# Kernel tuning notes

Measured on AMD Instinct MI355X. Metric: run time of the kernel, lower is better.

Reference implementation:

```python
import jax, jax.numpy as jnp
import numpy as np


def setup_inputs() -> dict:
    key = jax.random.key(0)
    k1, k2, k3 = jax.random.split(key, 3)
    B, S, D = 4, 2048, 1024   # batch, seq_len, hidden
    M = 65536                 # external memory size
    x = jax.random.normal(k1, (B, S, D), dtype=jnp.float32)
    keys = jax.random.normal(k2, (M, D), dtype=jnp.float32)
    vals = jax.random.normal(k3, (M, D), dtype=jnp.float32)
    return {"x": x, "ver": 1, "keys": keys, "vals": vals}


def reference(x, ver, keys, vals):
    # linear_attention: unnormalized attention over external memory.
    #   out = (x @ keys^T) @ vals
    # Use associativity to avoid materializing the [B,S,M] score matrix:
    #   kv = keys^T @ vals  -> [D, D]
    kv = jnp.einsum("md,me->de", keys, vals)   # [D, D]
    out = jnp.einsum("bsd,de->bse", x, kv)      # [B, S, D]
    return out
```

## Files before the change

### kernel.cpp

```cpp
#include <hip/hip_runtime.h>
#include <hip/hip_bf16.h>


typedef __attribute__((ext_vector_type(8))) __bf16 bf16x8;
typedef __attribute__((ext_vector_type(4))) __bf16 bf16x4;
typedef __attribute__((ext_vector_type(4))) float  f32x4;

#define D_DIM   1024
#define M_DIM   65536
#define ROWS    8192
#define NCHUNK  16
#define MC      (M_DIM / NCHUNK)
#define BT      128
#define BK      64
#define LDK     72
#define TILE_BYTES 16384

__device__ __forceinline__ f32x4 mfma16(bf16x8 a, bf16x8 b, f32x4 c) {
    return __builtin_amdgcn_mfma_f32_16x16x32_bf16(a, b, c, 0, 0, 0);
}

__device__ __forceinline__ void gl_lds16(const void* gsrc, void* ldst) {
    __builtin_amdgcn_global_load_lds(
        (const __attribute__((address_space(1))) unsigned int*)gsrc,
        (__attribute__((address_space(3))) unsigned int*)ldst,
        16, 0, 0);
}

__global__ __launch_bounds__(256)
void convert_tile(const float* __restrict__ keys,
                  const float* __restrict__ vals,
                  __hip_bfloat16* __restrict__ KtT,
                  __hip_bfloat16* __restrict__ VtT)
{
    __shared__ __bf16 Lt[128][72];

    const float* src = blockIdx.z ? vals : keys;
    char* dstb = (char*)(blockIdx.z ? VtT : KtT);

    const int tid = threadIdx.x;
    const int s  = blockIdx.x;
    const int t  = blockIdx.y;
    const int m0 = s * 64;
    const int d0 = t * 128;

    #pragma unroll
    for (int i = 0; i < 8; ++i) {
        const int idx = tid + i * 256;
        const int mr  = idx >> 5;
        const int dc  = (idx & 31) * 4;
        f32x4 v = *(const f32x4*)(src + (size_t)(m0 + mr) * D_DIM + d0 + dc);
        #pragma unroll
        for (int j = 0; j < 4; ++j)
            Lt[dc + j][mr] = (__bf16)v[j];
    }
    __syncthreads();

    char* dst_tile = dstb + ((size_t)t * 1024 + s) * TILE_BYTES;
    #pragma unroll
    for (int r = 0; r < 4; ++r) {
        const int o  = r * 4096 + tid * 16;
        const int dl = o >> 7;
        const int c  = (o >> 4) & 7;
        const int cl = c ^ (dl & 7);
        bf16x8 w = *(const bf16x8*)&Lt[dl][cl * 8];
        *(bf16x8*)(dst_tile + o) = w;
    }
}

__global__ __launch_bounds__(256)
void kv_gemm(const __hip_bfloat16* __restrict__ VtT,
             const __hip_bfloat16* __restrict__ KtT,
             float* __restrict__ kvw)
{
    __shared__ __bf16 Va[128][64];
    __shared__ __bf16 Ka[128][64];

    const int tid  = threadIdx.x;
    const int lane = tid & 63;
    const int wave = tid >> 6;
    const int wr   = wave >> 1;
    const int wc   = wave & 1;

    const int i64   = blockIdx.x & 63;
    const int chunk = blockIdx.x >> 6;
    const int xcd   = i64 & 7;
    const int slot  = i64 >> 3;
    const int e8 = (xcd >> 1) * 2 + (slot >> 2);
    const int d8 = (xcd & 1) * 4 + (slot & 3);

    const char* srcV = (const char*)VtT
        + ((size_t)e8 * 1024 + (size_t)chunk * 64) * TILE_BYTES
        + wave * 4096 + lane * 16;
    const char* srcK = (const char*)KtT
        + ((size_t)d8 * 1024 + (size_t)chunk * 64) * TILE_BYTES
        + wave * 4096 + lane * 16;
    char* dstV = (char*)&Va[0][0] + wave * 4096;
    char* dstK = (char*)&Ka[0][0] + wave * 4096;

    f32x4 acc[4][4] = {};

    const int l15 = lane & 15;
    const int l7  = lane & 7;
    const int hi  = lane >> 4;

    for (int it = 0; it < 64; ++it) {
        #pragma unroll
        for (int i = 0; i < 4; ++i) {
            gl_lds16(srcV + i * 1024, dstV + i * 1024);
            gl_lds16(srcK + i * 1024, dstK + i * 1024);
        }
        __syncthreads();

        const char* vbase = (const char*)&Va[0][0];
        const char* kbase = (const char*)&Ka[0][0];
        #pragma unroll
        for (int ks = 0; ks < BK; ks += 32) {
            bf16x8 af[4], bf[4];
            const int ca = (ks >> 3) + hi;
            const int pc = (ca ^ l7) << 4;
            #pragma unroll
            for (int tt = 0; tt < 4; ++tt) {
                const int ra = wr * 64 + tt * 16 + l15;
                const int rb = wc * 64 + tt * 16 + l15;
                af[tt] = *(const bf16x8*)(vbase + ra * 128 + pc);
                bf[tt] = *(const bf16x8*)(kbase + rb * 128 + pc);
            }
            #pragma unroll
            for (int mi = 0; mi < 4; ++mi)
                #pragma unroll
                for (int ni = 0; ni < 4; ++ni)
                    acc[mi][ni] = mfma16(af[mi], bf[ni], acc[mi][ni]);
        }
        __syncthreads();

        srcV += TILE_BYTES;
        srcK += TILE_BYTES;
    }

    const int rbase = (lane >> 4) * 4;
    const int cidx  = lane & 15;
    #pragma unroll
    for (int mi = 0; mi < 4; ++mi) {
        #pragma unroll
        for (int ni = 0; ni < 4; ++ni) {
            const int d = d8 * BT + wc * 64 + ni * 16 + cidx;
            #pragma unroll
            for (int reg = 0; reg < 4; ++reg) {
                const int e = e8 * BT + wr * 64 + mi * 16 + rbase + reg;
                atomicAdd(kvw + (size_t)e * D_DIM + d, acc[mi][ni][reg]);
            }
        }
    }
}

__global__ __launch_bounds__(256)
void kv_partial_kernel(const float* __restrict__ keys,
                       const float* __restrict__ vals,
                       float* __restrict__ kvw)
{
    __shared__ __bf16 Ktl[BT][LDK];
    __shared__ __bf16 Vtl[BT][LDK];

    const int tid  = threadIdx.x;
    const int lane = tid & 63;
    const int wave = tid >> 6;
    const int wr   = wave >> 1;
    const int wc   = wave & 1;

    const int tile  = blockIdx.x & 63;
    const int chunk = blockIdx.x >> 6;
    const int d0 = (tile >> 3) * BT;
    const int e0 = (tile & 7) * BT;
    const size_t mbeg = (size_t)chunk * MC;

    f32x4 acc[4][4] = {};
    const int kg  = tid & 15;
    const int d4a = tid >> 4;

    for (int ms = 0; ms < MC; ms += BK) {
        #pragma unroll
        for (int i = 0; i < 2; ++i) {
            const int dloc = (d4a + i * 16) * 4;
            const size_t mrow = mbeg + ms + (size_t)kg * 4;
            f32x4 kr[4], vr[4];
            #pragma unroll
            for (int r = 0; r < 4; ++r) {
                kr[r] = *(const f32x4*)(keys + (mrow + r) * D_DIM + d0 + dloc);
                vr[r] = *(const f32x4*)(vals + (mrow + r) * D_DIM + e0 + dloc);
            }
            #pragma unroll
            for (int j = 0; j < 4; ++j) {
                bf16x4 wk, wv;
                #pragma unroll
                for (int r = 0; r < 4; ++r) {
                    wk[r] = (__bf16)kr[r][j];
                    wv[r] = (__bf16)vr[r][j];
                }
                *(bf16x4*)&Ktl[dloc + j][kg * 4] = wk;
                *(bf16x4*)&Vtl[dloc + j][kg * 4] = wv;
            }
        }
        __syncthreads();

        #pragma unroll
        for (int ks = 0; ks < BK; ks += 32) {
            bf16x8 af[4], bf[4];
            #pragma unroll
            for (int t = 0; t < 4; ++t) {
                af[t] = *(const bf16x8*)&Ktl[wr * 64 + t * 16 + (lane & 15)][ks + (lane >> 4) * 8];
                bf[t] = *(const bf16x8*)&Vtl[wc * 64 + t * 16 + (lane & 15)][ks + (lane >> 4) * 8];
            }
            #pragma unroll
            for (int mi = 0; mi < 4; ++mi)
                #pragma unroll
                for (int ni = 0; ni < 4; ++ni)
                    acc[mi][ni] = mfma16(af[mi], bf[ni], acc[mi][ni]);
        }
        __syncthreads();
    }

    const int rbase = (lane >> 4) * 4;
    const int cidx  = lane & 15;
    #pragma unroll
    for (int mi = 0; mi < 4; ++mi) {
        #pragma unroll
        for (int ni = 0; ni < 4; ++ni) {
            const int e = e0 + wc * 64 + ni * 16 + cidx;
            #pragma unroll
            for (int reg = 0; reg < 4; ++reg) {
                const int d = d0 + wr * 64 + mi * 16 + rbase + reg;
                atomicAdd(kvw + (size_t)e * D_DIM + d, acc[mi][ni][reg]);
            }
        }
    }
}

__global__ __launch_bounds__(256)
void out_gemm_kernel(const float* __restrict__ x,
                     const float* __restrict__ kvw,
                     float* __restrict__ out)
{
    __shared__ __bf16 Xt[BT][LDK];
    __shared__ __bf16 Wt[BT][LDK];

    const int tid  = threadIdx.x;
    const int lane = tid & 63;
    const int wave = tid >> 6;
    const int wr   = wave >> 1;
    const int wc   = wave & 1;

    const int r0 = blockIdx.x * BT;
    const int e0 = blockIdx.y * BT;

    f32x4 acc[4][4] = {};

    for (int ks0 = 0; ks0 < D_DIM; ks0 += BK) {
        #pragma unroll
        for (int i = 0; i < 8; ++i) {
            const int idx = tid + i * 256;
            const int row = idx >> 4;
            const int col = (idx & 15) * 4;
            f32x4 xa = *(const f32x4*)(x   + (size_t)(r0 + row) * D_DIM + ks0 + col);
            f32x4 wa = *(const f32x4*)(kvw + (size_t)(e0 + row) * D_DIM + ks0 + col);
            bf16x4 xb, wb;
            #pragma unroll
            for (int j = 0; j < 4; ++j) {
                xb[j] = (__bf16)xa[j];
                wb[j] = (__bf16)wa[j];
            }
            *(bf16x4*)&Xt[row][col] = xb;
            *(bf16x4*)&Wt[row][col] = wb;
        }
        __syncthreads();

        #pragma unroll
        for (int ks = 0; ks < BK; ks += 32) {
            bf16x8 af[4], bf[4];
            #pragma unroll
            for (int t = 0; t < 4; ++t) {
                af[t] = *(const bf16x8*)&Xt[wr * 64 + t * 16 + (lane & 15)][ks + (lane >> 4) * 8];
                bf[t] = *(const bf16x8*)&Wt[wc * 64 + t * 16 + (lane & 15)][ks + (lane >> 4) * 8];
            }
            #pragma unroll
            for (int mi = 0; mi < 4; ++mi)
                #pragma unroll
                for (int ni = 0; ni < 4; ++ni)
                    acc[mi][ni] = mfma16(af[mi], bf[ni], acc[mi][ni]);
        }
        __syncthreads();
    }

    const int rbase = (lane >> 4) * 4;
    const int cidx  = lane & 15;
    #pragma unroll
    for (int mi = 0; mi < 4; ++mi) {
        #pragma unroll
        for (int ni = 0; ni < 4; ++ni) {
            const int e = e0 + wc * 64 + ni * 16 + cidx;
            #pragma unroll
            for (int reg = 0; reg < 4; ++reg) {
                const int r = r0 + wr * 64 + mi * 16 + rbase + reg;
                out[(size_t)r * D_DIM + e] = acc[mi][ni][reg];
            }
        }
    }
}

extern "C" void kernel_launch(void* const* d_in, const int* in_sizes, int n_in,
                              void* d_out, int out_size, void* d_ws, size_t ws_size,
                              hipStream_t stream) {
    const float* x    = (const float*)d_in[0];
    const float* keys = (const float*)d_in[2];
    const float* vals = (const float*)d_in[3];
    float* out = (float*)d_out;

    const size_t kvw_bytes = (size_t)D_DIM * D_DIM * sizeof(float);
    const size_t kt_bytes  = (size_t)D_DIM * M_DIM * sizeof(__hip_bfloat16);
    const size_t need      = kvw_bytes + 2 * kt_bytes;

    float* kvw = (float*)d_ws;
    hipMemsetAsync(kvw, 0, kvw_bytes, stream);

    if (ws_size >= need) {
        __hip_bfloat16* KtT = (__hip_bfloat16*)((char*)d_ws + kvw_bytes);
        __hip_bfloat16* VtT = (__hip_bfloat16*)((char*)d_ws + kvw_bytes + kt_bytes);
        convert_tile<<<dim3(M_DIM / 64, D_DIM / 128, 2), dim3(256), 0, stream>>>(
            keys, vals, KtT, VtT);
        kv_gemm<<<dim3(64 * NCHUNK), dim3(256), 0, stream>>>(VtT, KtT, kvw);
    } else {
        kv_partial_kernel<<<dim3(64 * NCHUNK), dim3(256), 0, stream>>>(keys, vals, kvw);
    }
    out_gemm_kernel<<<dim3(64, 8), dim3(256), 0, stream>>>(x, kvw, out);
}
```

Before: 425.9 us.

## Double-buffer LDS tiles in kv_gemm to overlap global loads with MFMA

Shared-memory tiles for V and K are doubled so the next K-step's global-to-LDS loads are issued before computing on the current buffer. A partial vmcnt wait (allowing the 8 newest loads in flight) plus raw s_barrier replaces the full __syncthreads, aiming to hide memory latency behind MFMA work. This doubles LDS use to 64 KB per block, which may reduce occupancy. Correctness relies on hand-written waitcnt and barrier ordering.

```diff
diff --git a/kernel.cpp b/kernel.cpp
--- a/kernel.cpp
+++ b/kernel.cpp
@@ -73,8 +73,8 @@
              const __hip_bfloat16* __restrict__ KtT,
              float* __restrict__ kvw)
 {
-    __shared__ __bf16 Va[128][64];
-    __shared__ __bf16 Ka[128][64];
+    __shared__ __bf16 Va[2][128][64];
+    __shared__ __bf16 Ka[2][128][64];
 
     const int tid  = threadIdx.x;
     const int lane = tid & 63;
@@ -95,8 +95,6 @@
     const char* srcK = (const char*)KtT
         + ((size_t)d8 * 1024 + (size_t)chunk * 64) * TILE_BYTES
         + wave * 4096 + lane * 16;
-    char* dstV = (char*)&Va[0][0] + wave * 4096;
-    char* dstK = (char*)&Ka[0][0] + wave * 4096;
 
     f32x4 acc[4][4] = {};
 
@@ -104,16 +102,31 @@
     const int l7  = lane & 7;
     const int hi  = lane >> 4;
 
-    for (int it = 0; it < 64; ++it) {
+    auto stage = [&](int buf, int t) {
+        const char* sv = srcV + (size_t)t * TILE_BYTES;
+        const char* sk = srcK + (size_t)t * TILE_BYTES;
+        char* dv = (char*)&Va[buf][0][0] + wave * 4096;
+        char* dk = (char*)&Ka[buf][0][0] + wave * 4096;
         #pragma unroll
         for (int i = 0; i < 4; ++i) {
-            gl_lds16(srcV + i * 1024, dstV + i * 1024);
-            gl_lds16(srcK + i * 1024, dstK + i * 1024);
-        }
-        __syncthreads();
-
-        const char* vbase = (const char*)&Va[0][0];
-        const char* kbase = (const char*)&Ka[0][0];
+            gl_lds16(sv + i * 1024, dv + i * 1024);
+            gl_lds16(sk + i * 1024, dk + i * 1024);
+        }
+    };
+
+    stage(0, 0);
+
+    for (int t = 0; t < 64; ++t) {
+        if (t + 1 < 64) {
+            stage((t + 1) & 1, t + 1);
+            asm volatile("s_waitcnt vmcnt(8)" ::: "memory");
+        } else {
+            asm volatile("s_waitcnt vmcnt(0)" ::: "memory");
+        }
+        __builtin_amdgcn_s_barrier();
+
+        const char* vbase = (const char*)&Va[t & 1][0][0];
+        const char* kbase = (const char*)&Ka[t & 1][0][0];
         #pragma unroll
         for (int ks = 0; ks < BK; ks += 32) {
             bf16x8 af[4], bf[4];
@@ -132,10 +145,7 @@
                 for (int ni = 0; ni < 4; ++ni)
                     acc[mi][ni] = mfma16(af[mi], bf[ni], acc[mi][ni]);
         }
-        __syncthreads();
-
-        srcV += TILE_BYTES;
-        srcK += TILE_BYTES;
+        __builtin_amdgcn_s_barrier();
     }
 
     const int rbase = (lane >> 4) * 4;
```

After: 437.5 us. 2.7% more time.
